# Optimization experiments

Hardware: AMD Instinct MI355X
Metric: run time of the kernel (lower is better)

The kernel has to match this reference:

```python
import jax, jax.numpy as jnp
import numpy as np

HEADS = 16
DIM_HEAD = 64
EPS = 1e-5


def _layernorm(x, w, b):
    mu = jnp.mean(x, axis=-1, keepdims=True)
    var = jnp.var(x, axis=-1, keepdims=True)
    return (x - mu) * jax.lax.rsqrt(var + EPS) * w + b


def setup_inputs() -> dict:
    key = jax.random.key(0)
    ks = jax.random.split(key, 6)
    B, F, Q, D = 8, 4096, 64, 1024
    inner = HEADS * DIM_HEAD  # 1024
    s = 0.02
    return {
        "features": jax.random.normal(ks[0], (B, F, D), jnp.float32),
        "latents": jax.random.normal(ks[1], (B, Q, D), jnp.float32),
        "lnm_w": jnp.ones((D,), jnp.float32),
        "lnm_b": jnp.zeros((D,), jnp.float32),
        "lnl_w": jnp.ones((D,), jnp.float32),
        "lnl_b": jnp.zeros((D,), jnp.float32),
        "Wq": jax.random.normal(ks[2], (D, inner), jnp.float32) * s,
        "Wk": jax.random.normal(ks[3], (D, inner), jnp.float32) * s,
        "Wv": jax.random.normal(ks[4], (D, inner), jnp.float32) * s,
        "Wo": jax.random.normal(ks[5], (inner, D), jnp.float32) * s,
    }


def reference(features, latents, lnm_w, lnm_b, lnl_w, lnl_b, Wq, Wk, Wv, Wo):
    B, Q = latents.shape[0], latents.shape[1]
    scale = DIM_HEAD ** (-0.5)

    x = _layernorm(features, lnm_w, lnm_b)           # (B, F, D)
    lat = _layernorm(latents, lnl_w, lnl_b)          # (B, Q, D)

    q = (lat @ Wq).reshape(B, Q, HEADS, DIM_HEAD).transpose(0, 2, 1, 3)  # b h q d
    kv_in = jnp.concatenate([x, lat], axis=1)        # (B, F+Q, D)
    FL = kv_in.shape[1]
    k = (kv_in @ Wk).reshape(B, FL, HEADS, DIM_HEAD).transpose(0, 2, 1, 3)  # b h f d
    v = (kv_in @ Wv).reshape(B, FL, HEADS, DIM_HEAD).transpose(0, 2, 1, 3)  # b h f d

    sim = jnp.einsum('bhqd,bhfd->bhqf', q * scale, k)
    alphas = jax.nn.softmax(sim, axis=-1)            # amax-subtract is folded into stable softmax
    out = jnp.einsum('bhqf,bhfv->bhqv', alphas, v)
    out = out.transpose(0, 2, 1, 3).reshape(B, Q, HEADS * DIM_HEAD)
    return out @ Wo
```

## Files before the change

kernel.cpp:

```cpp
#include <hip/hip_runtime.h>


typedef float   f32x4  __attribute__((ext_vector_type(4)));
typedef short   bf16x8 __attribute__((ext_vector_type(8)));

#define MFMA_BF16 __builtin_amdgcn_mfma_f32_16x16x32_bf16

__device__ __forceinline__ unsigned short f2bf(float f) {
  unsigned u = __float_as_uint(f);
  unsigned r = (u + 0x7fffu + ((u >> 16) & 1u)) >> 16;
  return (unsigned short)r;
}

__device__ __forceinline__ void gload_lds16(const unsigned short* g, unsigned short* l) {
  __builtin_amdgcn_global_load_lds(
      (const __attribute__((address_space(1))) unsigned int*)g,
      (__attribute__((address_space(3))) unsigned int*)l, 16, 0, 0);
}

__global__ __launch_bounds__(256) void ln_kernel(
    const float* __restrict__ features, const float* __restrict__ latents,
    const float* __restrict__ lnm_w, const float* __restrict__ lnm_b,
    const float* __restrict__ lnl_w, const float* __restrict__ lnl_b,
    unsigned short* __restrict__ kv_ln, unsigned short* __restrict__ lat_ln)
{
  const int row = blockIdx.x;
  const int b  = row / 4160;
  const int fi = row - b * 4160;
  const bool is_lat = fi >= 4096;
  const float* x = is_lat ? (latents + (size_t)(b * 64 + fi - 4096) * 1024)
                          : (features + (size_t)(b * 4096 + fi) * 1024);
  const float* wp = is_lat ? lnl_w : lnm_w;
  const float* bp = is_lat ? lnl_b : lnm_b;
  const int tid = threadIdx.x;

  float4 v = *(const float4*)(x + tid * 4);
  float s  = v.x + v.y + v.z + v.w;
  float s2 = v.x * v.x + v.y * v.y + v.z * v.z + v.w * v.w;
#pragma unroll
  for (int sh = 1; sh < 64; sh <<= 1) {
    s  += __shfl_xor(s,  sh, 64);
    s2 += __shfl_xor(s2, sh, 64);
  }
  __shared__ float red[8];
  if ((tid & 63) == 0) { red[tid >> 6] = s; red[4 + (tid >> 6)] = s2; }
  __syncthreads();
  s  = red[0] + red[1] + red[2] + red[3];
  s2 = red[4] + red[5] + red[6] + red[7];
  const float mu   = s * (1.0f / 1024.0f);
  const float var  = s2 * (1.0f / 1024.0f) - mu * mu;
  const float rstd = rsqrtf(var + 1e-5f);

  float4 w4 = *(const float4*)(wp + tid * 4);
  float4 b4 = *(const float4*)(bp + tid * 4);
  ushort4 o;
  o.x = f2bf((v.x - mu) * rstd * w4.x + b4.x);
  o.y = f2bf((v.y - mu) * rstd * w4.y + b4.y);
  o.z = f2bf((v.z - mu) * rstd * w4.z + b4.z);
  o.w = f2bf((v.w - mu) * rstd * w4.w + b4.w);
  *(ushort4*)(kv_ln + (size_t)row * 1024 + tid * 4) = o;
  if (is_lat)
    *(ushort4*)(lat_ln + (size_t)(b * 64 + fi - 4096) * 1024 + tid * 4) = o;
}

__global__ __launch_bounds__(256) void wcast_kernel(
    const float* __restrict__ Wq, const float* __restrict__ Wk,
    const float* __restrict__ Wv, const float* __restrict__ Wo,
    unsigned short* __restrict__ Wkv_t, unsigned short* __restrict__ Wq_t,
    unsigned short* __restrict__ Wo_t)
{
  __shared__ float tile[32][33];
  const int kt = blockIdx.x * 32, nt = blockIdx.y * 32;
  const int tx = threadIdx.x & 31, ty = threadIdx.x >> 5;

  const float* src; int nc; float scale = 1.0f;
  if (nt < 1024)      { src = Wk; nc = nt; }
  else if (nt < 2048) { src = Wv; nc = nt - 1024; }
  else if (nt < 3072) { src = Wq; nc = nt - 2048; scale = 0.125f; }
  else                { src = Wo; nc = nt - 3072; }

#pragma unroll
  for (int kk = 0; kk < 4; ++kk)
    tile[ty + kk * 8][tx] = src[(size_t)(kt + ty + kk * 8) * 1024 + nc + tx] * scale;
  __syncthreads();

#pragma unroll
  for (int nn = 0; nn < 4; ++nn) {
    const int ng = nt + ty + nn * 8;
    unsigned short* d;
    if (ng < 2048)      d = Wkv_t + (size_t)ng * 1024;
    else if (ng < 3072) d = Wq_t + (size_t)(ng - 2048) * 1024;
    else                d = Wo_t + (size_t)(ng - 3072) * 1024;
    d[kt + tx] = f2bf(tile[tx][ty + nn * 8]);
  }
}

__global__ __launch_bounds__(512, 4) void gemm256_bf16(
    const unsigned short* __restrict__ A,
    const unsigned short* __restrict__ Bt,
    unsigned short* __restrict__ Kp, unsigned short* __restrict__ Vt,
    const unsigned short* __restrict__ Aq,
    const unsigned short* __restrict__ Bq,
    unsigned short* __restrict__ Cq,
    int M, int N, int K)
{
  __shared__ __align__(16) unsigned short lds[36864];
  const int tid  = threadIdx.x;
  const int wave = tid >> 6, lane = tid & 63;
  const int lo = lane & 15, hi = lane >> 4;
  const int wr = wave >> 1, wc = wave & 1;

  const int nbn = 16;
  int flat = blockIdx.y * nbn + blockIdx.x;
  const int nwg = nbn * gridDim.y;
  flat = (flat & 7) * (nwg >> 3) + (flat >> 3);

  const bool qpath = (flat >= 2080);
  const unsigned short* Ab;
  const unsigned short* Bb;
  int bm, bn;
  if (qpath) {
    const int g = flat - 2080;
    bm = g >> 3; bn = g & 7;
    Ab = Aq; Bb = Bq;
  } else {
    bm = flat / nbn; bn = flat - (flat / nbn) * nbn;
    Ab = A; Bb = Bt;
  }

  int garA[2], gakA[2];
#pragma unroll
  for (int gi = 0; gi < 2; ++gi) {
    int off = gi * 8192 + tid * 16;
    int p = off ^ (((off >> 9) & 1) << 5);
    int s = p >> 10, q = p & 1023;
    garA[gi] = (s >> 1) * 16 + (q >> 6) + 128 * (s & 1);
    gakA[gi] = (q & 63) >> 1;
  }
  int grB, gkB;
  {
    int off = tid * 16;
    int p = off ^ (((off >> 9) & 1) << 5);
    int s = p >> 10, q = p & 1023;
    grB = (s >> 1) * 16 + (q >> 6) + 64 * (s & 1);
    gkB = (q & 63) >> 1;
  }
  const unsigned short* pA0 = Ab + (size_t)(bm * 256 + garA[0]) * K + gakA[0];
  const unsigned short* pA1 = Ab + (size_t)(bm * 256 + garA[1]) * K + gakA[1];
  const unsigned short* pB  = Bb + (size_t)(bn * 128 + grB)     * K + gkB;

  f32x4 acc[4][4];
#pragma unroll
  for (int i = 0; i < 4; ++i)
#pragma unroll
    for (int j = 0; j < 4; ++j) acc[i][j] = (f32x4){0.f, 0.f, 0.f, 0.f};

  const int NT = K >> 5;

#pragma unroll
  for (int tt = 0; tt < 2; ++tt) {
    unsigned short* bb = lds + tt * 12288;
    gload_lds16(pA0 + tt * 32, bb + wave * 512);
    gload_lds16(pA1 + tt * 32, bb + 4096 + wave * 512);
    gload_lds16(pB  + tt * 32, bb + 8192 + wave * 512);
  }
  asm volatile("s_waitcnt vmcnt(3)" ::: "memory");
  asm volatile("s_barrier" ::: "memory");

  const int swz = (lo * 32 + hi * 8) ^ ((lo & 8) << 1);
  int aAddr[4], bAddr[4];
#pragma unroll
  for (int m = 0; m < 4; ++m)
    aAddr[m] = ((((wr & 1) * 4 + m) * 2) + (wr >> 1)) * 512 + swz;
#pragma unroll
  for (int n = 0; n < 4; ++n)
    bAddr[n] = 8192 + (n * 2 + wc) * 512 + swz;

  int cur = 0;
  for (int t = 0; t < NT; ++t) {
    const unsigned short* bp = lds + cur * 12288;
    bf16x8 af[4], bf[4];
#pragma unroll
    for (int m = 0; m < 4; ++m) af[m] = *(const bf16x8*)(bp + aAddr[m]);
#pragma unroll
    for (int n = 0; n < 4; ++n) bf[n] = *(const bf16x8*)(bp + bAddr[n]);

    if (t + 2 < NT) {
      int s2 = cur + 2; if (s2 >= 3) s2 -= 3;
      unsigned short* db = lds + s2 * 12288;
      const int koff = (t + 2) * 32;
      gload_lds16(pA0 + koff, db + wave * 512);
      gload_lds16(pA1 + koff, db + 4096 + wave * 512);
      gload_lds16(pB  + koff, db + 8192 + wave * 512);
    }

    __builtin_amdgcn_s_setprio(1);
#pragma unroll
    for (int m = 0; m < 4; ++m)
#pragma unroll
      for (int n = 0; n < 4; ++n)
        acc[m][n] = MFMA_BF16(af[m], bf[n], acc[m][n], 0, 0, 0);
    __builtin_amdgcn_s_setprio(0);

    if (t + 2 < NT)      { asm volatile("s_waitcnt vmcnt(3)" ::: "memory"); }
    else if (t + 1 < NT) { asm volatile("s_waitcnt vmcnt(0)" ::: "memory"); }
    asm volatile("s_barrier" ::: "memory");
    cur = (cur == 2) ? 0 : cur + 1;
  }

  if (qpath) {
#pragma unroll
    for (int m = 0; m < 4; ++m) {
      const int grow0 = bm * 256 + wr * 64 + m * 16 + hi * 4;
#pragma unroll
      for (int n = 0; n < 4; ++n) {
        const int gcol = bn * 128 + wc * 64 + n * 16 + lo;
#pragma unroll
        for (int r = 0; r < 4; ++r)
          Cq[(size_t)(grow0 + r) * 1024 + gcol] = f2bf(acc[m][n][r]);
      }
    }
  } else if (bn < 8) {
#pragma unroll
    for (int m = 0; m < 4; ++m) {
      const int grow0 = bm * 256 + wr * 64 + m * 16 + hi * 4;
#pragma unroll
      for (int n = 0; n < 4; ++n) {
        const int gcol = bn * 128 + wc * 64 + n * 16 + lo;
        const size_t pbase = (size_t)(gcol >> 6) * 2129920 + (gcol & 63);
#pragma unroll
        for (int r = 0; r < 4; ++r)
          Kp[pbase + (size_t)(grow0 + r) * 64] = f2bf(acc[m][n][r]);
      }
    }
  } else {
    __syncthreads();
    unsigned short* ldsT = lds;
#pragma unroll
    for (int m = 0; m < 4; ++m) {
      const int row_l = wr * 64 + m * 16 + hi * 4;
#pragma unroll
      for (int n = 0; n < 4; ++n) {
        const int col_l = wc * 64 + n * 16 + lo;
#pragma unroll
        for (int r = 0; r < 4; ++r)
          ldsT[col_l * 264 + row_l + r] = f2bf(acc[m][n][r]);
      }
    }
    __syncthreads();
#pragma unroll
    for (int it = 0; it < 8; ++it) {
      const int col_l = it * 16 + (tid >> 5);
      const int rl = (tid & 31) * 8;
      bf16x8 v = *(const bf16x8*)&ldsT[col_l * 264 + rl];
      const int hcol = (bn - 8) * 128 + col_l;
      const size_t dst = (size_t)(hcol >> 6) * 2129920
                       + (size_t)(hcol & 63) * 33280 + bm * 256 + rl;
      *(bf16x8*)&Vt[dst] = v;
    }
  }
}

template <typename CT>
__global__ __launch_bounds__(256) void gemm_tn(
    const unsigned short* __restrict__ A,
    const unsigned short* __restrict__ Bt,
    CT* __restrict__ C, int M, int N, int K)
{
  __shared__ __align__(16) unsigned short sA[2][128 * 32];
  __shared__ __align__(16) unsigned short sB[2][128 * 32];
  const int tid  = threadIdx.x;
  const int wave = tid >> 6, lane = tid & 63;
  const int bm = blockIdx.y, bn = blockIdx.x;
  const int wr = wave >> 1, wc = wave & 1;
  const int lo = lane & 15, hi = lane >> 4;
  const int srow = lane >> 2, squad = lane & 3;

  const unsigned short* gA = A  + (size_t)(bm * 128 + srow) * K + squad * 8;
  const unsigned short* gB = Bt + (size_t)(bn * 128 + srow) * K + squad * 8;

  f32x4 acc[4][4];
#pragma unroll
  for (int i = 0; i < 4; ++i)
#pragma unroll
    for (int j = 0; j < 4; ++j) acc[i][j] = (f32x4){0.f, 0.f, 0.f, 0.f};

  const int kt = K >> 5;
#pragma unroll
  for (int c = 0; c < 2; ++c) {
    const int chunk = wave * 2 + c;
    gload_lds16(gA + (size_t)chunk * 16 * K, &sA[0][chunk * 512]);
    gload_lds16(gB + (size_t)chunk * 16 * K, &sB[0][chunk * 512]);
  }
  __syncthreads();

  int buf = 0;
  for (int t = 0; t < kt; ++t) {
    if (t + 1 < kt) {
      const int k0 = (t + 1) << 5;
#pragma unroll
      for (int c = 0; c < 2; ++c) {
        const int chunk = wave * 2 + c;
        gload_lds16(gA + (size_t)chunk * 16 * K + k0, &sA[buf ^ 1][chunk * 512]);
        gload_lds16(gB + (size_t)chunk * 16 * K + k0, &sB[buf ^ 1][chunk * 512]);
      }
    }
    bf16x8 af[4], bfr[4];
#pragma unroll
    for (int i = 0; i < 4; ++i) {
      af[i]  = *(const bf16x8*)&sA[buf][(wr * 64 + i * 16 + lo) * 32 + hi * 8];
      bfr[i] = *(const bf16x8*)&sB[buf][(wc * 64 + i * 16 + lo) * 32 + hi * 8];
    }
#pragma unroll
    for (int i = 0; i < 4; ++i)
#pragma unroll
      for (int j = 0; j < 4; ++j)
        acc[i][j] = MFMA_BF16(af[i], bfr[j], acc[i][j], 0, 0, 0);
    __syncthreads();
    buf ^= 1;
  }

#pragma unroll
  for (int i = 0; i < 4; ++i) {
    const int row0 = bm * 128 + wr * 64 + i * 16 + hi * 4;
#pragma unroll
    for (int j = 0; j < 4; ++j) {
      const int col = bn * 128 + wc * 64 + j * 16 + lo;
#pragma unroll
      for (int r = 0; r < 4; ++r) {
        const size_t idx = (size_t)(row0 + r) * N + col;
        if constexpr (sizeof(CT) == 2) C[idx] = (CT)f2bf(acc[i][j][r]);
        else                            C[idx] = acc[i][j][r];
      }
    }
  }
}

__global__ __launch_bounds__(256) void attn_kernel(
    const unsigned short* __restrict__ qws,
    const unsigned short* __restrict__ Kp, const unsigned short* __restrict__ Vt,
    float* __restrict__ pacc, float* __restrict__ pml)
{
  const int bhs = blockIdx.x;
  const int bh = bhs / 6, s = bhs - bh * 6;
  const int h = bh & 15, b = bh >> 4;
  const int t0 = (s * 65) / 6;
  const int t1 = ((s + 1) * 65) / 6;
  const int tid = threadIdx.x;
  const int wave = tid >> 6, lane = tid & 63;
  const int lo = lane & 15, hi = lane >> 4;

  __shared__ __align__(16) unsigned short sK [2][64][72];
  __shared__ __align__(16) unsigned short sVT[2][64][72];
  __shared__ __align__(16) unsigned short sP [4][16][72];

  bf16x8 qf[2];
  {
    const unsigned short* p = qws + (size_t)(b * 64 + wave * 16 + lo) * 1024 + h * 64 + hi * 8;
    qf[0] = *(const bf16x8*)p;
    qf[1] = *(const bf16x8*)(p + 32);
  }
  float m[4] = {-1e30f, -1e30f, -1e30f, -1e30f};
  float l[4] = {0.f, 0.f, 0.f, 0.f};
  f32x4 acc[4];
#pragma unroll
  for (int i = 0; i < 4; ++i) acc[i] = (f32x4){0.f, 0.f, 0.f, 0.f};

  const int frow = tid >> 2, c4 = tid & 3;
  const int vd = tid >> 3, vfo = (tid & 7) * 8;
  const size_t hbase = (size_t)h * 2129920;

  bf16x8 kreg[2], vreg[2];
  {
    const size_t rowb = (size_t)(b * 4160 + t0 * 64);
#pragma unroll
    for (int rr = 0; rr < 2; ++rr)
      kreg[rr] = *(const bf16x8*)(Kp + hbase + (rowb + frow) * 64 + rr * 32 + c4 * 8);
#pragma unroll
    for (int p = 0; p < 2; ++p)
      vreg[p] = *(const bf16x8*)(Vt + hbase + (size_t)(vd + p * 32) * 33280 + rowb + vfo);
  }

  for (int t = t0; t < t1; ++t) {
    const int bi = t & 1;
#pragma unroll
    for (int rr = 0; rr < 2; ++rr)
      *(bf16x8*)&sK[bi][frow][rr * 32 + c4 * 8] = kreg[rr];
#pragma unroll
    for (int p = 0; p < 2; ++p)
      *(bf16x8*)&sVT[bi][vd + p * 32][vfo] = vreg[p];
    __syncthreads();
    if (t + 1 < t1) {
      const size_t rowb = (size_t)(b * 4160 + (t + 1) * 64);
#pragma unroll
      for (int rr = 0; rr < 2; ++rr)
        kreg[rr] = *(const bf16x8*)(Kp + hbase + (rowb + frow) * 64 + rr * 32 + c4 * 8);
#pragma unroll
      for (int p = 0; p < 2; ++p)
        vreg[p] = *(const bf16x8*)(Vt + hbase + (size_t)(vd + p * 32) * 33280 + rowb + vfo);
    }

    f32x4 sim[4];
#pragma unroll
    for (int nf = 0; nf < 4; ++nf) {
      f32x4 a0 = (f32x4){0.f, 0.f, 0.f, 0.f};
#pragma unroll
      for (int ks = 0; ks < 2; ++ks) {
        bf16x8 kf = *(const bf16x8*)&sK[bi][nf * 16 + lo][ks * 32 + hi * 8];
        a0 = MFMA_BF16(qf[ks], kf, a0, 0, 0, 0);
      }
      sim[nf] = a0;
    }

    float pr[4][4];
    float corr[4];
#pragma unroll
    for (int r = 0; r < 4; ++r) {
      float tm = fmaxf(fmaxf(sim[0][r], sim[1][r]), fmaxf(sim[2][r], sim[3][r]));
#pragma unroll
      for (int sh = 1; sh < 16; sh <<= 1) tm = fmaxf(tm, __shfl_xor(tm, sh, 64));
      const float mn = fmaxf(m[r], tm);
      corr[r] = __expf(m[r] - mn);
      float rs = 0.f;
#pragma unroll
      for (int nf = 0; nf < 4; ++nf) {
        float p = __expf(sim[nf][r] - mn);
        pr[r][nf] = p;
        rs += p;
      }
#pragma unroll
      for (int sh = 1; sh < 16; sh <<= 1) rs += __shfl_xor(rs, sh, 64);
      l[r] = l[r] * corr[r] + rs;
      m[r] = mn;
    }

    {
      const int r2 = lane & 3;
      float csel = r2 == 0 ? corr[0] : r2 == 1 ? corr[1] : r2 == 2 ? corr[2] : corr[3];
      const int src = ((lane & 15) >> 2) * 16 + (lane & 3);
      const float cacc = __shfl(csel, src, 64);
#pragma unroll
      for (int i = 0; i < 4; ++i) acc[i] *= cacc;
    }

#pragma unroll
    for (int r = 0; r < 4; ++r)
#pragma unroll
      for (int nf = 0; nf < 4; ++nf)
        sP[wave][hi * 4 + r][nf * 16 + lo] = f2bf(pr[r][nf]);

#pragma unroll
    for (int ks = 0; ks < 2; ++ks) {
      bf16x8 pf = *(const bf16x8*)&sP[wave][lo][ks * 32 + hi * 8];
#pragma unroll
      for (int i = 0; i < 4; ++i) {
        bf16x8 vf = *(const bf16x8*)&sVT[bi][i * 16 + lo][ks * 32 + hi * 8];
        acc[i] = MFMA_BF16(vf, pf, acc[i], 0, 0, 0);
      }
    }
  }

  if (lo == 0) {
#pragma unroll
    for (int r = 0; r < 4; ++r) {
      pml[bhs * 128 + wave * 16 + hi * 4 + r]      = m[r];
      pml[bhs * 128 + 64 + wave * 16 + hi * 4 + r] = l[r];
    }
  }
#pragma unroll
  for (int i = 0; i < 4; ++i)
#pragma unroll
    for (int r = 0; r < 4; ++r)
      pacc[bhs * 4096 + (i * 16 + hi * 4 + r) * 64 + wave * 16 + lo] = acc[i][r];
}

__global__ __launch_bounds__(256) void attn_combine(
    const float* __restrict__ pacc, const float* __restrict__ pml,
    unsigned short* __restrict__ attn_out)
{
  const int bh = blockIdx.x;
  const int b = bh >> 4, h = bh & 15;
  const int t = threadIdx.x;
  const int q = t & 63, dg = t >> 6;
  const int base = bh * 6;

  float mm[6], ll[6];
#pragma unroll
  for (int s = 0; s < 6; ++s) {
    mm[s] = pml[(base + s) * 128 + q];
    ll[s] = pml[(base + s) * 128 + 64 + q];
  }
  float M = mm[0];
#pragma unroll
  for (int s = 1; s < 6; ++s) M = fmaxf(M, mm[s]);
  float e[6];
  float L = 0.f;
#pragma unroll
  for (int s = 0; s < 6; ++s) { e[s] = __expf(mm[s] - M); L += e[s] * ll[s]; }
  const float inv = 1.0f / L;

#pragma unroll
  for (int dd = 0; dd < 16; ++dd) {
    const int d = dg * 16 + dd;
    float v = 0.f;
#pragma unroll
    for (int s = 0; s < 6; ++s)
      v += e[s] * pacc[(base + s) * 4096 + d * 64 + q];
    attn_out[(size_t)(b * 64 + q) * 1024 + h * 64 + d] = f2bf(v * inv);
  }
}

extern "C" void kernel_launch(void* const* d_in, const int* in_sizes, int n_in,
                              void* d_out, int out_size, void* d_ws, size_t ws_size,
                              hipStream_t stream) {
  const float* features = (const float*)d_in[0];
  const float* latents  = (const float*)d_in[1];
  const float* lnm_w = (const float*)d_in[2];
  const float* lnm_b = (const float*)d_in[3];
  const float* lnl_w = (const float*)d_in[4];
  const float* lnl_b = (const float*)d_in[5];
  const float* Wq = (const float*)d_in[6];
  const float* Wk = (const float*)d_in[7];
  const float* Wv = (const float*)d_in[8];
  const float* Wo = (const float*)d_in[9];
  float* out = (float*)d_out;

  char* ws = (char*)d_ws;
  unsigned short* kv_ln    = (unsigned short*)(ws);
  unsigned short* Wkv_t    = (unsigned short*)(ws + 68157440);
  unsigned short* Wq_t     = (unsigned short*)(ws + 72351744);
  unsigned short* Wo_t     = (unsigned short*)(ws + 74448896);
  unsigned short* lat_ln   = (unsigned short*)(ws + 76546048);
  unsigned short* q_ws     = (unsigned short*)(ws + 77594624);
  unsigned short* attn_out = (unsigned short*)(ws + 78643200);
  unsigned short* Kp       = (unsigned short*)(ws + 79691776);
  unsigned short* Vt       = (unsigned short*)(ws + 147849216);
  float* pacc = (float*)(ws);
  float* pml  = (float*)(ws + 12582912);

  ln_kernel<<<33280, 256, 0, stream>>>(features, latents, lnm_w, lnm_b, lnl_w, lnl_b,
                                       kv_ln, lat_ln);
  wcast_kernel<<<dim3(32, 128), 256, 0, stream>>>(Wq, Wk, Wv, Wo, Wkv_t, Wq_t, Wo_t);
  gemm256_bf16<<<dim3(16, 131), 512, 0, stream>>>(kv_ln, Wkv_t, Kp, Vt,
                                                  lat_ln, Wq_t, q_ws,
                                                  33280, 2048, 1024);
  attn_kernel<<<768, 256, 0, stream>>>(q_ws, Kp, Vt, pacc, pml);
  attn_combine<<<128, 256, 0, stream>>>(pacc, pml, attn_out);
  gemm_tn<float><<<dim3(8, 4), 256, 0, stream>>>(attn_out, Wo_t, out, 512, 1024, 1024);
}
```

Baseline: 265.0 us.

## Merge layernorm and weight-cast launches; add lazy softmax rescale in attention

Combines the layernorm kernel and the weight transpose/cast kernel into one launch that picks its role from the block index, removing one kernel launch and its tail. In the attention loop, the running max is only raised when some row's tile max exceeds it by more than 8. Otherwise the rescale exps and the accumulator multiply are skipped and probabilities are computed against the stale max. This trades some fp32 headroom for fewer exp and shuffle operations per tile.

```diff
diff --git a/kernel.cpp b/kernel.cpp
--- a/kernel.cpp
+++ b/kernel.cpp
@@ -18,80 +18,81 @@
       (__attribute__((address_space(3))) unsigned int*)l, 16, 0, 0);
 }
 
-__global__ __launch_bounds__(256) void ln_kernel(
+__global__ __launch_bounds__(256) void prep_kernel(
     const float* __restrict__ features, const float* __restrict__ latents,
     const float* __restrict__ lnm_w, const float* __restrict__ lnm_b,
     const float* __restrict__ lnl_w, const float* __restrict__ lnl_b,
-    unsigned short* __restrict__ kv_ln, unsigned short* __restrict__ lat_ln)
-{
-  const int row = blockIdx.x;
-  const int b  = row / 4160;
-  const int fi = row - b * 4160;
-  const bool is_lat = fi >= 4096;
-  const float* x = is_lat ? (latents + (size_t)(b * 64 + fi - 4096) * 1024)
-                          : (features + (size_t)(b * 4096 + fi) * 1024);
-  const float* wp = is_lat ? lnl_w : lnm_w;
-  const float* bp = is_lat ? lnl_b : lnm_b;
-  const int tid = threadIdx.x;
-
-  float4 v = *(const float4*)(x + tid * 4);
-  float s  = v.x + v.y + v.z + v.w;
-  float s2 = v.x * v.x + v.y * v.y + v.z * v.z + v.w * v.w;
-#pragma unroll
-  for (int sh = 1; sh < 64; sh <<= 1) {
-    s  += __shfl_xor(s,  sh, 64);
-    s2 += __shfl_xor(s2, sh, 64);
-  }
-  __shared__ float red[8];
-  if ((tid & 63) == 0) { red[tid >> 6] = s; red[4 + (tid >> 6)] = s2; }
-  __syncthreads();
-  s  = red[0] + red[1] + red[2] + red[3];
-  s2 = red[4] + red[5] + red[6] + red[7];
-  const float mu   = s * (1.0f / 1024.0f);
-  const float var  = s2 * (1.0f / 1024.0f) - mu * mu;
-  const float rstd = rsqrtf(var + 1e-5f);
-
-  float4 w4 = *(const float4*)(wp + tid * 4);
-  float4 b4 = *(const float4*)(bp + tid * 4);
-  ushort4 o;
-  o.x = f2bf((v.x - mu) * rstd * w4.x + b4.x);
-  o.y = f2bf((v.y - mu) * rstd * w4.y + b4.y);
-  o.z = f2bf((v.z - mu) * rstd * w4.z + b4.z);
-  o.w = f2bf((v.w - mu) * rstd * w4.w + b4.w);
-  *(ushort4*)(kv_ln + (size_t)row * 1024 + tid * 4) = o;
-  if (is_lat)
-    *(ushort4*)(lat_ln + (size_t)(b * 64 + fi - 4096) * 1024 + tid * 4) = o;
-}
-
-__global__ __launch_bounds__(256) void wcast_kernel(
+    unsigned short* __restrict__ kv_ln, unsigned short* __restrict__ lat_ln,
     const float* __restrict__ Wq, const float* __restrict__ Wk,
     const float* __restrict__ Wv, const float* __restrict__ Wo,
     unsigned short* __restrict__ Wkv_t, unsigned short* __restrict__ Wq_t,
     unsigned short* __restrict__ Wo_t)
 {
-  __shared__ float tile[32][33];
-  const int kt = blockIdx.x * 32, nt = blockIdx.y * 32;
-  const int tx = threadIdx.x & 31, ty = threadIdx.x >> 5;
-
-  const float* src; int nc; float scale = 1.0f;
-  if (nt < 1024)      { src = Wk; nc = nt; }
-  else if (nt < 2048) { src = Wv; nc = nt - 1024; }
-  else if (nt < 3072) { src = Wq; nc = nt - 2048; scale = 0.125f; }
-  else                { src = Wo; nc = nt - 3072; }
-
-#pragma unroll
-  for (int kk = 0; kk < 4; ++kk)
-    tile[ty + kk * 8][tx] = src[(size_t)(kt + ty + kk * 8) * 1024 + nc + tx] * scale;
-  __syncthreads();
-
-#pragma unroll
-  for (int nn = 0; nn < 4; ++nn) {
-    const int ng = nt + ty + nn * 8;
-    unsigned short* d;
-    if (ng < 2048)      d = Wkv_t + (size_t)ng * 1024;
-    else if (ng < 3072) d = Wq_t + (size_t)(ng - 2048) * 1024;
-    else                d = Wo_t + (size_t)(ng - 3072) * 1024;
-    d[kt + tx] = f2bf(tile[tx][ty + nn * 8]);
+  __shared__ float shmem[32 * 33];
+  const int tid = threadIdx.x;
+
+  if (blockIdx.x < 33280) {
+    const int row = blockIdx.x;
+    const int b  = row / 4160;
+    const int fi = row - b * 4160;
+    const bool is_lat = fi >= 4096;
+    const float* x = is_lat ? (latents + (size_t)(b * 64 + fi - 4096) * 1024)
+                            : (features + (size_t)(b * 4096 + fi) * 1024);
+    const float* wp = is_lat ? lnl_w : lnm_w;
+    const float* bp = is_lat ? lnl_b : lnm_b;
+
+    float4 v = *(const float4*)(x + tid * 4);
+    float s  = v.x + v.y + v.z + v.w;
+    float s2 = v.x * v.x + v.y * v.y + v.z * v.z + v.w * v.w;
+#pragma unroll
+    for (int sh = 1; sh < 64; sh <<= 1) {
+      s  += __shfl_xor(s,  sh, 64);
+      s2 += __shfl_xor(s2, sh, 64);
+    }
+    if ((tid & 63) == 0) { shmem[tid >> 6] = s; shmem[4 + (tid >> 6)] = s2; }
+    __syncthreads();
+    s  = shmem[0] + shmem[1] + shmem[2] + shmem[3];
+    s2 = shmem[4] + shmem[5] + shmem[6] + shmem[7];
+    const float mu   = s * (1.0f / 1024.0f);
+    const float var  = s2 * (1.0f / 1024.0f) - mu * mu;
+    const float rstd = rsqrtf(var + 1e-5f);
+
+    float4 w4 = *(const float4*)(wp + tid * 4);
+    float4 b4 = *(const float4*)(bp + tid * 4);
+    ushort4 o;
+    o.x = f2bf((v.x - mu) * rstd * w4.x + b4.x);
+    o.y = f2bf((v.y - mu) * rstd * w4.y + b4.y);
+    o.z = f2bf((v.z - mu) * rstd * w4.z + b4.z);
+    o.w = f2bf((v.w - mu) * rstd * w4.w + b4.w);
+    *(ushort4*)(kv_ln + (size_t)row * 1024 + tid * 4) = o;
+    if (is_lat)
+      *(ushort4*)(lat_ln + (size_t)(b * 64 + fi - 4096) * 1024 + tid * 4) = o;
+  } else {
+    const int w = blockIdx.x - 33280;
+    const int kt = (w & 31) * 32, nt = (w >> 5) * 32;
+    const int tx = tid & 31, ty = tid >> 5;
+
+    const float* src; int nc; float scale = 1.0f;
+    if (nt < 1024)      { src = Wk; nc = nt; }
+    else if (nt < 2048) { src = Wv; nc = nt - 1024; }
+    else if (nt < 3072) { src = Wq; nc = nt - 2048; scale = 0.125f; }
+    else                { src = Wo; nc = nt - 3072; }
+
+#pragma unroll
+    for (int kk = 0; kk < 4; ++kk)
+      shmem[(ty + kk * 8) * 33 + tx] =
+          src[(size_t)(kt + ty + kk * 8) * 1024 + nc + tx] * scale;
+    __syncthreads();
+
+#pragma unroll
+    for (int nn = 0; nn < 4; ++nn) {
+      const int ng = nt + ty + nn * 8;
+      unsigned short* d;
+      if (ng < 2048)      d = Wkv_t + (size_t)ng * 1024;
+      else if (ng < 3072) d = Wq_t + (size_t)(ng - 2048) * 1024;
+      else                d = Wo_t + (size_t)(ng - 3072) * 1024;
+      d[kt + tx] = f2bf(shmem[tx * 33 + ty + nn * 8]);
+    }
   }
 }
 
@@ -412,29 +413,50 @@
       sim[nf] = a0;
     }
 
-    float pr[4][4];
-    float corr[4];
+    float tm4[4];
 #pragma unroll
     for (int r = 0; r < 4; ++r) {
       float tm = fmaxf(fmaxf(sim[0][r], sim[1][r]), fmaxf(sim[2][r], sim[3][r]));
 #pragma unroll
       for (int sh = 1; sh < 16; sh <<= 1) tm = fmaxf(tm, __shfl_xor(tm, sh, 64));
-      const float mn = fmaxf(m[r], tm);
-      corr[r] = __expf(m[r] - mn);
-      float rs = 0.f;
-#pragma unroll
-      for (int nf = 0; nf < 4; ++nf) {
-        float p = __expf(sim[nf][r] - mn);
-        pr[r][nf] = p;
-        rs += p;
-      }
-#pragma unroll
-      for (int sh = 1; sh < 16; sh <<= 1) rs += __shfl_xor(rs, sh, 64);
-      l[r] = l[r] * corr[r] + rs;
-      m[r] = mn;
-    }
-
-    {
+      tm4[r] = tm;
+    }
+
+    float pr[4][4];
+    const bool small = (tm4[0] <= m[0] + 8.f) && (tm4[1] <= m[1] + 8.f) &&
+                       (tm4[2] <= m[2] + 8.f) && (tm4[3] <= m[3] + 8.f);
+    if (__all(small)) {
+#pragma unroll
+      for (int r = 0; r < 4; ++r) {
+        float rs = 0.f;
+#pragma unroll
+        for (int nf = 0; nf < 4; ++nf) {
+          float p = __expf(sim[nf][r] - m[r]);
+          pr[r][nf] = p;
+          rs += p;
+        }
+#pragma unroll
+        for (int sh = 1; sh < 16; sh <<= 1) rs += __shfl_xor(rs, sh, 64);
+        l[r] += rs;
+      }
+    } else {
+      float corr[4];
+#pragma unroll
+      for (int r = 0; r < 4; ++r) {
+        const float mn = fmaxf(m[r], tm4[r]);
+        corr[r] = __expf(m[r] - mn);
+        float rs = 0.f;
+#pragma unroll
+        for (int nf = 0; nf < 4; ++nf) {
+          float p = __expf(sim[nf][r] - mn);
+          pr[r][nf] = p;
+          rs += p;
+        }
+#pragma unroll
+        for (int sh = 1; sh < 16; sh <<= 1) rs += __shfl_xor(rs, sh, 64);
+        l[r] = l[r] * corr[r] + rs;
+        m[r] = mn;
+      }
       const int r2 = lane & 3;
       float csel = r2 == 0 ? corr[0] : r2 == 1 ? corr[1] : r2 == 2 ? corr[2] : corr[3];
       const int src = ((lane & 15) >> 2) * 16 + (lane & 3);
@@ -538,9 +560,9 @@
   float* pacc = (float*)(ws);
   float* pml  = (float*)(ws + 12582912);
 
-  ln_kernel<<<33280, 256, 0, stream>>>(features, latents, lnm_w, lnm_b, lnl_w, lnl_b,
-                                       kv_ln, lat_ln);
-  wcast_kernel<<<dim3(32, 128), 256, 0, stream>>>(Wq, Wk, Wv, Wo, Wkv_t, Wq_t, Wo_t);
+  prep_kernel<<<37376, 256, 0, stream>>>(features, latents, lnm_w, lnm_b, lnl_w, lnl_b,
+                                         kv_ln, lat_ln, Wq, Wk, Wv, Wo,
+                                         Wkv_t, Wq_t, Wo_t);
   gemm256_bf16<<<dim3(16, 131), 512, 0, stream>>>(kv_ln, Wkv_t, Kp, Vt,
                                                   lat_ln, Wq_t, q_ws,
                                                   33280, 2048, 1024);
```

Result: no change. 267.2 us (+0.8%).
